# Performance work log

Hardware: AMD Instinct MI355X
Metric: run time of the kernel (lower is better)

## Reference

```python
import jax, jax.numpy as jnp
import numpy as np

NUM_NODE = 50000
NUM_REL = 50
NUM_EDGE = 1_000_000
NUM_TRI = 2_000_000
HIDDEN = 64


def setup_inputs() -> dict:
    key = jax.random.key(0)
    ks = jax.random.split(key, 9)
    rel_emb = jax.random.normal(ks[0], (NUM_REL, HIDDEN), dtype=jnp.float32)
    W_msg = jax.random.normal(ks[1], (2 * HIDDEN, HIDDEN), dtype=jnp.float32) / np.sqrt(2 * HIDDEN)
    W_upd = jax.random.normal(ks[2], (2 * HIDDEN, HIDDEN), dtype=jnp.float32) / np.sqrt(2 * HIDDEN)
    src = jax.random.randint(ks[3], (NUM_EDGE,), 0, NUM_NODE, dtype=jnp.int64 if jax.config.jax_enable_x64 else jnp.int32)
    dst = jax.random.randint(ks[4], (NUM_EDGE,), 0, NUM_NODE, dtype=src.dtype)
    rel = jax.random.randint(ks[5], (NUM_EDGE,), 0, NUM_REL, dtype=src.dtype)
    edge_ab = jax.random.randint(ks[6], (NUM_TRI,), 0, NUM_EDGE, dtype=src.dtype)
    edge_bc = jax.random.randint(ks[7], (NUM_TRI,), 0, NUM_EDGE, dtype=src.dtype)
    edge_ac = jax.random.randint(ks[8], (NUM_TRI,), 0, NUM_EDGE, dtype=src.dtype)
    return {
        "rel_emb": rel_emb, "W_msg": W_msg, "W_upd": W_upd,
        "src": src, "dst": dst, "rel": rel,
        "edge_ab": edge_ab, "edge_bc": edge_bc, "edge_ac": edge_ac,
    }


def reference(rel_emb, W_msg, W_upd, src, dst, rel, edge_ab, edge_bc, edge_ac):
    # Per-edge hidden state from relation embedding: [E, D]
    h = rel_emb[rel]
    num_edge = h.shape[0]
    # Triangle message: combine the two body edges of each grounding. [T, 2D]
    pair = jnp.concatenate([h[edge_ab], h[edge_bc]], axis=-1)
    msg = jax.nn.relu(pair @ W_msg)  # [T, D]
    # Scatter-add messages onto the head edge (a,c): irregular, memory-bound.
    agg = jax.ops.segment_sum(msg, edge_ac, num_segments=num_edge)  # [E, D]
    # Edge update.
    out = jax.nn.relu(jnp.concatenate([h, agg], axis=-1) @ W_upd)  # [E, D]
    return out
```

## Files before the change

kernel.cpp:

```cpp
#include <hip/hip_runtime.h>

#define HIDDEN 64
#define NREL 50
#define NPAIR (NREL * NREL)
#define BEDGE 64
#define CAP 512

typedef int   iv4 __attribute__((ext_vector_type(4)));
typedef float fv4 __attribute__((ext_vector_type(4)));

__global__ void precompute_tables(const float* __restrict__ rel_emb,
                                  const float* __restrict__ W_msg,
                                  const float* __restrict__ W_upd,
                                  const int* __restrict__ rel,
                                  unsigned char* __restrict__ rel8,
                                  int conv_n,
                                  float* __restrict__ M2,
                                  float* __restrict__ Hc) {
    const int p = blockIdx.x;
    const int j = threadIdx.x;

    for (int i = p * HIDDEN + j; i < conv_n; i += NPAIR * HIDDEN)
        rel8[i] = (unsigned char)rel[i];

    const int ra = p / NREL, rb = p % NREL;
    __shared__ float msg[HIDDEN];
    const float* ha = rel_emb + ra * HIDDEN;
    const float* hb = rel_emb + rb * HIDDEN;

    float acc = 0.f;
    #pragma unroll 8
    for (int i = 0; i < HIDDEN; ++i) acc += ha[i] * W_msg[i * HIDDEN + j];
    #pragma unroll 8
    for (int i = 0; i < HIDDEN; ++i) acc += hb[i] * W_msg[(HIDDEN + i) * HIDDEN + j];
    msg[j] = fmaxf(acc, 0.f);
    __syncthreads();

    float acc2 = 0.f;
    #pragma unroll 8
    for (int k = 0; k < HIDDEN; ++k) acc2 += msg[k] * W_upd[(HIDDEN + k) * HIDDEN + j];
    M2[p * HIDDEN + j] = acc2;

    if (p < NREL) {
        float acc3 = 0.f;
        #pragma unroll 8
        for (int i = 0; i < HIDDEN; ++i) acc3 += rel_emb[p * HIDDEN + i] * W_upd[i * HIDDEN + j];
        Hc[p * HIDDEN + j] = acc3;
    }
}

__global__ __launch_bounds__(256) void partition_tri(
        const unsigned char* __restrict__ rel8,
        const int* __restrict__ edge_ab,
        const int* __restrict__ edge_bc,
        const int* __restrict__ edge_ac,
        unsigned int* __restrict__ cur,
        unsigned int* __restrict__ buf,
        int num_tri) {
    const int n8 = num_tri >> 3;
    int i = blockIdx.x * blockDim.x + threadIdx.x;
    const int stride = gridDim.x * blockDim.x;
    for (; i < n8; i += stride) {
        const iv4 a0 = __builtin_nontemporal_load((const iv4*)edge_ab + 2 * i);
        const iv4 a1 = __builtin_nontemporal_load((const iv4*)edge_ab + 2 * i + 1);
        const iv4 b0 = __builtin_nontemporal_load((const iv4*)edge_bc + 2 * i);
        const iv4 b1 = __builtin_nontemporal_load((const iv4*)edge_bc + 2 * i + 1);
        const iv4 c0 = __builtin_nontemporal_load((const iv4*)edge_ac + 2 * i);
        const iv4 c1 = __builtin_nontemporal_load((const iv4*)edge_ac + 2 * i + 1);
        int p[8], c[8];
        #pragma unroll
        for (int k = 0; k < 4; ++k) {
            p[k]     = (int)rel8[a0[k]] * NREL + (int)rel8[b0[k]];
            p[k + 4] = (int)rel8[a1[k]] * NREL + (int)rel8[b1[k]];
            c[k]     = c0[k];
            c[k + 4] = c1[k];
        }
        unsigned int r[8];
        #pragma unroll
        for (int k = 0; k < 8; ++k)
            r[k] = atomicAdd(&cur[c[k] >> 6], 1u);
        #pragma unroll
        for (int k = 0; k < 8; ++k)
            if (r[k] < CAP)
                buf[(size_t)(c[k] >> 6) * CAP + r[k]] =
                    ((unsigned int)p[k] << 6) | ((unsigned int)c[k] & 63u);
    }
    const int rem = num_tri & 7;
    if (rem && blockIdx.x == gridDim.x - 1 && threadIdx.x < rem) {
        const int t = (num_tri & ~7) + threadIdx.x;
        const int p = (int)rel8[edge_ab[t]] * NREL + (int)rel8[edge_bc[t]];
        const int c = edge_ac[t];
        const unsigned int r = atomicAdd(&cur[c >> 6], 1u);
        if (r < CAP)
            buf[(size_t)(c >> 6) * CAP + r] =
                ((unsigned int)p << 6) | ((unsigned int)c & 63u);
    }
}

__global__ __launch_bounds__(256) void accumulate_bucket(
        const unsigned char* __restrict__ rel8,
        const unsigned int* __restrict__ cur,
        const unsigned int* __restrict__ buf,
        const float* __restrict__ M2,
        const float* __restrict__ Hc,
        float* __restrict__ out, int num_edge) {
    __shared__ unsigned int lk[CAP];
    const int b = blockIdx.x;
    const unsigned int craw = cur[b];
    const int cnt = craw < CAP ? (int)craw : CAP;
    for (int t = threadIdx.x; t < cnt; t += 256)
        lk[t] = buf[(size_t)b * CAP + t];
    __syncthreads();

    const int g     = threadIdx.x >> 4;
    const int l     = threadIdx.x & 15;
    const int shift = threadIdx.x & 48;

    for (int le = g; le < BEDGE; le += 16) {
        const int e = b * BEDGE + le;
        if (e >= num_edge) continue;
        const int re = rel8[e];
        fv4 acc = ((const fv4*)(Hc + re * HIDDEN))[l];
        for (int base = 0; base < cnt; base += 16) {
            const int idx = base + l;
            const unsigned int key = (idx < cnt) ? lk[idx] : 0u;
            const bool m = (idx < cnt) && ((int)(key & 63u) == le);
            const unsigned long long bal = __ballot(m);
            unsigned int mask = (unsigned int)((bal >> shift) & 0xFFFFull);
            while (mask) {
                const int bit = __ffs(mask) - 1;
                mask &= mask - 1;
                const int p = __shfl((int)(key >> 6), bit, 16);
                acc += ((const fv4*)M2)[p * 16 + l];
            }
        }
        fv4 o = acc;
        o.x = fmaxf(o.x, 0.f);
        o.y = fmaxf(o.y, 0.f);
        o.z = fmaxf(o.z, 0.f);
        o.w = fmaxf(o.w, 0.f);
        __builtin_nontemporal_store(o, (fv4*)out + (size_t)e * 16 + l);
    }
}

__global__ void scatter_tri(const int* __restrict__ rel,
                            const int* __restrict__ edge_ab,
                            const int* __restrict__ edge_bc,
                            const int* __restrict__ edge_ac,
                            const float* __restrict__ M2,
                            float* __restrict__ out, int num_tri) {
    const int lane   = threadIdx.x & 63;
    const int wave   = (int)((blockIdx.x * blockDim.x + threadIdx.x) >> 6);
    const int nwaves = (int)((gridDim.x * blockDim.x) >> 6);
    for (int t = wave; t < num_tri; t += nwaves) {
        const int p = rel[edge_ab[t]] * NREL + rel[edge_bc[t]];
        const float v = M2[p * HIDDEN + lane];
        unsafeAtomicAdd(&out[(size_t)edge_ac[t] * HIDDEN + lane], v);
    }
}

__global__ void finalize(const int* __restrict__ rel,
                         const float* __restrict__ Hc,
                         float* __restrict__ out, int num_edge) {
    const int total = num_edge * (HIDDEN / 4);
    int i = blockIdx.x * blockDim.x + threadIdx.x;
    const int stride = gridDim.x * blockDim.x;
    for (; i < total; i += stride) {
        const int e = i >> 4;
        const int q = i & 15;
        float4 a = ((const float4*)out)[i];
        float4 h = ((const float4*)(Hc + rel[e] * HIDDEN))[q];
        float4 o;
        o.x = fmaxf(a.x + h.x, 0.f);
        o.y = fmaxf(a.y + h.y, 0.f);
        o.z = fmaxf(a.z + h.z, 0.f);
        o.w = fmaxf(a.w + h.w, 0.f);
        ((float4*)out)[i] = o;
    }
}

extern "C" void kernel_launch(void* const* d_in, const int* in_sizes, int n_in,
                              void* d_out, int out_size, void* d_ws, size_t ws_size,
                              hipStream_t stream) {
    const float* rel_emb = (const float*)d_in[0];
    const float* W_msg   = (const float*)d_in[1];
    const float* W_upd   = (const float*)d_in[2];
    const int* rel     = (const int*)d_in[5];
    const int* edge_ab = (const int*)d_in[6];
    const int* edge_bc = (const int*)d_in[7];
    const int* edge_ac = (const int*)d_in[8];
    float* out = (float*)d_out;

    const int num_edge = in_sizes[5];
    const int num_tri  = in_sizes[6];
    const int NB = (num_edge + BEDGE - 1) / BEDGE;

    char* ws = (char*)d_ws;
    size_t off = 0;
    auto alloc = [&](size_t bytes) { char* p = ws + off; off = (off + bytes + 255) & ~(size_t)255; return p; };
    float*         M2   = (float*)alloc((size_t)NPAIR * HIDDEN * 4);
    float*         Hc   = (float*)alloc((size_t)NREL * HIDDEN * 4);
    unsigned char* rel8 = (unsigned char*)alloc((size_t)num_edge);
    unsigned int*  cur  = (unsigned int*)alloc((size_t)NB * 4);
    unsigned int*  buf  = (unsigned int*)alloc((size_t)NB * CAP * 4);
    const size_t required = off;

    const bool fast = (ws_size >= required);

    if (fast) {
        hipMemsetAsync(cur, 0, (size_t)NB * 4, stream);
        precompute_tables<<<NPAIR, HIDDEN, 0, stream>>>(rel_emb, W_msg, W_upd,
                                                        rel, rel8, num_edge, M2, Hc);
        const int n8 = num_tri >> 3;
        int pblocks = (n8 + 255) / 256;
        if (pblocks < 1) pblocks = 1;
        partition_tri<<<pblocks, 256, 0, stream>>>(rel8, edge_ab, edge_bc, edge_ac,
                                                   cur, buf, num_tri);
        accumulate_bucket<<<NB, 256, 0, stream>>>(rel8, cur, buf, M2, Hc,
                                                  out, num_edge);
    } else {
        precompute_tables<<<NPAIR, HIDDEN, 0, stream>>>(rel_emb, W_msg, W_upd,
                                                        rel, (unsigned char*)d_ws, 0, M2, Hc);
        hipMemsetAsync(d_out, 0, (size_t)out_size * sizeof(float), stream);
        scatter_tri<<<8192, 256, 0, stream>>>(rel, edge_ab, edge_bc, edge_ac, M2, out, num_tri);
        const int total4 = num_edge * (HIDDEN / 4);
        int fin_blocks = (total4 + 255) / 256;
        if (fin_blocks > 65535 * 8) fin_blocks = 65535 * 8;
        finalize<<<fin_blocks, 256, 0, stream>>>(rel, Hc, out, num_edge);
    }
}
```

Baseline: 465.4 us.

## Accumulate bucketed triangle messages with LDS atomics instead of ballot scans

The per-bucket accumulation kernel now keeps a padded shared-memory accumulator for all 64 edges in the bucket, seeded from the Hc table. Each group of 16 threads takes one bucketed key and adds the matching M2 row with LDS float atomics. This replaces the earlier scheme in which every edge group rescanned the whole key list with ballots and shuffles, doing work proportional to edges times keys. Bucket buffer writes and reads also switch to nontemporal accesses. The cost is a larger LDS footprint and contention among LDS atomics.

```diff
diff --git a/kernel.cpp b/kernel.cpp
--- a/kernel.cpp
+++ b/kernel.cpp
@@ -5,6 +5,7 @@
 #define NPAIR (NREL * NREL)
 #define BEDGE 64
 #define CAP 512
+#define AC_STRIDE 68
 
 typedef int   iv4 __attribute__((ext_vector_type(4)));
 typedef float fv4 __attribute__((ext_vector_type(4)));
@@ -82,8 +83,9 @@
         #pragma unroll
         for (int k = 0; k < 8; ++k)
             if (r[k] < CAP)
-                buf[(size_t)(c[k] >> 6) * CAP + r[k]] =
-                    ((unsigned int)p[k] << 6) | ((unsigned int)c[k] & 63u);
+                __builtin_nontemporal_store(
+                    ((unsigned int)p[k] << 6) | ((unsigned int)c[k] & 63u),
+                    &buf[(size_t)(c[k] >> 6) * CAP + r[k]]);
     }
     const int rem = num_tri & 7;
     if (rem && blockIdx.x == gridDim.x - 1 && threadIdx.x < rem) {
@@ -97,49 +99,54 @@
     }
 }
 
-__global__ __launch_bounds__(256) void accumulate_bucket(
+__global__ __launch_bounds__(256) void accumulate_lds(
         const unsigned char* __restrict__ rel8,
         const unsigned int* __restrict__ cur,
         const unsigned int* __restrict__ buf,
         const float* __restrict__ M2,
         const float* __restrict__ Hc,
         float* __restrict__ out, int num_edge) {
+    __shared__ float acc[BEDGE * AC_STRIDE];
     __shared__ unsigned int lk[CAP];
-    const int b = blockIdx.x;
+    const int b  = blockIdx.x;
+    const int e0 = b * BEDGE;
+    int ne = num_edge - e0;
+    if (ne > BEDGE) ne = BEDGE;
+
+    for (int idx = threadIdx.x; idx < ne * 16; idx += 256) {
+        const int le = idx >> 4, q = idx & 15;
+        const int re = rel8[e0 + le];
+        *(fv4*)(acc + le * AC_STRIDE + q * 4) = ((const fv4*)(Hc + re * HIDDEN))[q];
+    }
     const unsigned int craw = cur[b];
     const int cnt = craw < CAP ? (int)craw : CAP;
     for (int t = threadIdx.x; t < cnt; t += 256)
-        lk[t] = buf[(size_t)b * CAP + t];
+        lk[t] = __builtin_nontemporal_load(buf + (size_t)b * CAP + t);
     __syncthreads();
 
-    const int g     = threadIdx.x >> 4;
-    const int l     = threadIdx.x & 15;
-    const int shift = threadIdx.x & 48;
-
-    for (int le = g; le < BEDGE; le += 16) {
-        const int e = b * BEDGE + le;
-        if (e >= num_edge) continue;
-        const int re = rel8[e];
-        fv4 acc = ((const fv4*)(Hc + re * HIDDEN))[l];
-        for (int base = 0; base < cnt; base += 16) {
-            const int idx = base + l;
-            const unsigned int key = (idx < cnt) ? lk[idx] : 0u;
-            const bool m = (idx < cnt) && ((int)(key & 63u) == le);
-            const unsigned long long bal = __ballot(m);
-            unsigned int mask = (unsigned int)((bal >> shift) & 0xFFFFull);
-            while (mask) {
-                const int bit = __ffs(mask) - 1;
-                mask &= mask - 1;
-                const int p = __shfl((int)(key >> 6), bit, 16);
-                acc += ((const fv4*)M2)[p * 16 + l];
-            }
-        }
-        fv4 o = acc;
-        o.x = fmaxf(o.x, 0.f);
-        o.y = fmaxf(o.y, 0.f);
-        o.z = fmaxf(o.z, 0.f);
-        o.w = fmaxf(o.w, 0.f);
-        __builtin_nontemporal_store(o, (fv4*)out + (size_t)e * 16 + l);
+    const int g = threadIdx.x >> 4;
+    const int l = threadIdx.x & 15;
+    for (int kidx = g; kidx < cnt; kidx += 16) {
+        const unsigned int key = lk[kidx];
+        const int le = (int)(key & 63u);
+        const int p  = (int)(key >> 6);
+        const fv4 m = ((const fv4*)M2)[p * 16 + l];
+        float* dst = acc + le * AC_STRIDE + l * 4;
+        atomicAdd(dst + 0, m.x);
+        atomicAdd(dst + 1, m.y);
+        atomicAdd(dst + 2, m.z);
+        atomicAdd(dst + 3, m.w);
+    }
+    __syncthreads();
+
+    for (int idx = threadIdx.x; idx < ne * 16; idx += 256) {
+        const int le = idx >> 4, q = idx & 15;
+        fv4 v = *(const fv4*)(acc + le * AC_STRIDE + q * 4);
+        v.x = fmaxf(v.x, 0.f);
+        v.y = fmaxf(v.y, 0.f);
+        v.z = fmaxf(v.z, 0.f);
+        v.w = fmaxf(v.w, 0.f);
+        __builtin_nontemporal_store(v, (fv4*)out + (size_t)(e0 + le) * 16 + q);
     }
 }
 
@@ -216,8 +223,8 @@
         if (pblocks < 1) pblocks = 1;
         partition_tri<<<pblocks, 256, 0, stream>>>(rel8, edge_ab, edge_bc, edge_ac,
                                                    cur, buf, num_tri);
-        accumulate_bucket<<<NB, 256, 0, stream>>>(rel8, cur, buf, M2, Hc,
-                                                  out, num_edge);
+        accumulate_lds<<<NB, 256, 0, stream>>>(rel8, cur, buf, M2, Hc,
+                                               out, num_edge);
     } else {
         precompute_tables<<<NPAIR, HIDDEN, 0, stream>>>(rel_emb, W_msg, W_upd,
                                                         rel, (unsigned char*)d_ws, 0, M2, Hc);
```

Result: slower. 1.051 ms (+125.8%).

## Fuse precompute, partition and accumulate into one cooperative persistent kernel

Applied to the files above, without the earlier changes.

Replaces the memset plus three kernel launches with a single cooperative kernel. It zeroes counters, converts rel, builds the pair tables, partitions triangles into buckets and accumulates per-edge outputs, with grid-wide syncs between phases. The aim is to remove launch gaps and inter-kernel idle time. The cost is that a grid-sync barrier and a persistent grid capped at 2048 blocks may reduce latency hiding in the memory-bound phases. It falls back to the old multi-kernel path if the cooperative launch fails.

```diff
diff --git a/kernel.cpp b/kernel.cpp
--- a/kernel.cpp
+++ b/kernel.cpp
@@ -1,4 +1,7 @@
 #include <hip/hip_runtime.h>
+#include <hip/hip_cooperative_groups.h>
+
+namespace cg = cooperative_groups;
 
 #define HIDDEN 64
 #define NREL 50
@@ -8,6 +11,144 @@
 
 typedef int   iv4 __attribute__((ext_vector_type(4)));
 typedef float fv4 __attribute__((ext_vector_type(4)));
+
+__global__ __launch_bounds__(256) void fused_pipeline(
+        const float* __restrict__ rel_emb,
+        const float* __restrict__ W_msg,
+        const float* __restrict__ W_upd,
+        const int* __restrict__ rel,
+        const int* __restrict__ edge_ab,
+        const int* __restrict__ edge_bc,
+        const int* __restrict__ edge_ac,
+        unsigned char* __restrict__ rel8,
+        float* __restrict__ M2,
+        float* __restrict__ Hc,
+        unsigned int* __restrict__ cur,
+        unsigned int* __restrict__ buf,
+        float* __restrict__ out,
+        int num_edge, int num_tri, int NB_) {
+    cg::grid_group grid = cg::this_grid();
+    __shared__ float msg[4][HIDDEN];
+    __shared__ unsigned int lk[CAP];
+
+    const int tid      = threadIdx.x;
+    const int gtid     = blockIdx.x * blockDim.x + tid;
+    const int gthreads = gridDim.x * blockDim.x;
+
+    for (int i = gtid; i < NB_; i += gthreads) cur[i] = 0u;
+    for (int i = gtid; i < num_edge; i += gthreads) rel8[i] = (unsigned char)rel[i];
+
+    {
+        const int sub = tid >> 6;
+        const int j   = tid & 63;
+        const int pb  = blockIdx.x * 4 + sub;
+        if (pb < NPAIR) {
+            const int ra = pb / NREL, rb = pb % NREL;
+            const float* ha = rel_emb + ra * HIDDEN;
+            const float* hb = rel_emb + rb * HIDDEN;
+            float acc = 0.f;
+            #pragma unroll 8
+            for (int i = 0; i < HIDDEN; ++i) acc += ha[i] * W_msg[i * HIDDEN + j];
+            #pragma unroll 8
+            for (int i = 0; i < HIDDEN; ++i) acc += hb[i] * W_msg[(HIDDEN + i) * HIDDEN + j];
+            msg[sub][j] = fmaxf(acc, 0.f);
+            __syncthreads();
+            float acc2 = 0.f;
+            #pragma unroll 8
+            for (int k = 0; k < HIDDEN; ++k) acc2 += msg[sub][k] * W_upd[(HIDDEN + k) * HIDDEN + j];
+            M2[pb * HIDDEN + j] = acc2;
+            if (pb < NREL) {
+                float acc3 = 0.f;
+                #pragma unroll 8
+                for (int i = 0; i < HIDDEN; ++i) acc3 += rel_emb[pb * HIDDEN + i] * W_upd[i * HIDDEN + j];
+                Hc[pb * HIDDEN + j] = acc3;
+            }
+        }
+    }
+    grid.sync();
+
+    {
+        const int n8 = num_tri >> 3;
+        for (int i = gtid; i < n8; i += gthreads) {
+            const iv4 a0 = __builtin_nontemporal_load((const iv4*)edge_ab + 2 * i);
+            const iv4 a1 = __builtin_nontemporal_load((const iv4*)edge_ab + 2 * i + 1);
+            const iv4 b0 = __builtin_nontemporal_load((const iv4*)edge_bc + 2 * i);
+            const iv4 b1 = __builtin_nontemporal_load((const iv4*)edge_bc + 2 * i + 1);
+            const iv4 c0 = __builtin_nontemporal_load((const iv4*)edge_ac + 2 * i);
+            const iv4 c1 = __builtin_nontemporal_load((const iv4*)edge_ac + 2 * i + 1);
+            int p[8], c[8];
+            #pragma unroll
+            for (int k = 0; k < 4; ++k) {
+                p[k]     = (int)rel8[a0[k]] * NREL + (int)rel8[b0[k]];
+                p[k + 4] = (int)rel8[a1[k]] * NREL + (int)rel8[b1[k]];
+                c[k]     = c0[k];
+                c[k + 4] = c1[k];
+            }
+            unsigned int r[8];
+            #pragma unroll
+            for (int k = 0; k < 8; ++k)
+                r[k] = atomicAdd(&cur[c[k] >> 6], 1u);
+            #pragma unroll
+            for (int k = 0; k < 8; ++k)
+                if (r[k] < CAP)
+                    buf[(size_t)(c[k] >> 6) * CAP + r[k]] =
+                        ((unsigned int)p[k] << 6) | ((unsigned int)c[k] & 63u);
+        }
+        const int rem = num_tri & 7;
+        if (gtid < rem) {
+            const int t = (num_tri & ~7) + gtid;
+            const int p = (int)rel8[edge_ab[t]] * NREL + (int)rel8[edge_bc[t]];
+            const int c = edge_ac[t];
+            const unsigned int r = atomicAdd(&cur[c >> 6], 1u);
+            if (r < CAP)
+                buf[(size_t)(c >> 6) * CAP + r] =
+                    ((unsigned int)p << 6) | ((unsigned int)c & 63u);
+        }
+    }
+    grid.sync();
+
+    {
+        const int g     = tid >> 4;
+        const int l     = tid & 15;
+        const int shift = tid & 48;
+        for (int b = blockIdx.x; b < NB_; b += gridDim.x) {
+            const unsigned int craw = cur[b];
+            const int cnt = craw < CAP ? (int)craw : CAP;
+            for (int t = tid; t < cnt; t += 256)
+                lk[t] = buf[(size_t)b * CAP + t];
+            __syncthreads();
+
+            const int e0 = b * BEDGE;
+            for (int le = g; le < BEDGE; le += 16) {
+                const int e = e0 + le;
+                if (e < num_edge) {
+                    const int re = rel8[e];
+                    fv4 acc = ((const fv4*)(Hc + re * HIDDEN))[l];
+                    for (int base = 0; base < cnt; base += 16) {
+                        const int idx = base + l;
+                        const unsigned int key = (idx < cnt) ? lk[idx] : 0u;
+                        const bool m = (idx < cnt) && ((int)(key & 63u) == le);
+                        const unsigned long long bal = __ballot(m);
+                        unsigned int mask = (unsigned int)((bal >> shift) & 0xFFFFull);
+                        while (mask) {
+                            const int bit = __ffs(mask) - 1;
+                            mask &= mask - 1;
+                            const int p = __shfl((int)(key >> 6), bit, 16);
+                            acc += ((const fv4*)M2)[p * 16 + l];
+                        }
+                    }
+                    fv4 o = acc;
+                    o.x = fmaxf(o.x, 0.f);
+                    o.y = fmaxf(o.y, 0.f);
+                    o.z = fmaxf(o.z, 0.f);
+                    o.w = fmaxf(o.w, 0.f);
+                    __builtin_nontemporal_store(o, (fv4*)out + (size_t)e * 16 + l);
+                }
+            }
+            __syncthreads();
+        }
+    }
+}
 
 __global__ void precompute_tables(const float* __restrict__ rel_emb,
                                   const float* __restrict__ W_msg,
@@ -19,15 +160,12 @@
                                   float* __restrict__ Hc) {
     const int p = blockIdx.x;
     const int j = threadIdx.x;
-
     for (int i = p * HIDDEN + j; i < conv_n; i += NPAIR * HIDDEN)
         rel8[i] = (unsigned char)rel[i];
-
     const int ra = p / NREL, rb = p % NREL;
     __shared__ float msg[HIDDEN];
     const float* ha = rel_emb + ra * HIDDEN;
     const float* hb = rel_emb + rb * HIDDEN;
-
     float acc = 0.f;
     #pragma unroll 8
     for (int i = 0; i < HIDDEN; ++i) acc += ha[i] * W_msg[i * HIDDEN + j];
@@ -35,12 +173,10 @@
     for (int i = 0; i < HIDDEN; ++i) acc += hb[i] * W_msg[(HIDDEN + i) * HIDDEN + j];
     msg[j] = fmaxf(acc, 0.f);
     __syncthreads();
-
     float acc2 = 0.f;
     #pragma unroll 8
     for (int k = 0; k < HIDDEN; ++k) acc2 += msg[k] * W_upd[(HIDDEN + k) * HIDDEN + j];
     M2[p * HIDDEN + j] = acc2;
-
     if (p < NREL) {
         float acc3 = 0.f;
         #pragma unroll 8
@@ -111,11 +247,9 @@
     for (int t = threadIdx.x; t < cnt; t += 256)
         lk[t] = buf[(size_t)b * CAP + t];
     __syncthreads();
-
     const int g     = threadIdx.x >> 4;
     const int l     = threadIdx.x & 15;
     const int shift = threadIdx.x & 48;
-
     for (int le = g; le < BEDGE; le += 16) {
         const int e = b * BEDGE + le;
         if (e >= num_edge) continue;
@@ -193,7 +327,7 @@
 
     const int num_edge = in_sizes[5];
     const int num_tri  = in_sizes[6];
-    const int NB = (num_edge + BEDGE - 1) / BEDGE;
+    int NB = (num_edge + BEDGE - 1) / BEDGE;
 
     char* ws = (char*)d_ws;
     size_t off = 0;
@@ -205,19 +339,38 @@
     unsigned int*  buf  = (unsigned int*)alloc((size_t)NB * CAP * 4);
     const size_t required = off;
 
-    const bool fast = (ws_size >= required);
-
-    if (fast) {
-        hipMemsetAsync(cur, 0, (size_t)NB * 4, stream);
-        precompute_tables<<<NPAIR, HIDDEN, 0, stream>>>(rel_emb, W_msg, W_upd,
-                                                        rel, rel8, num_edge, M2, Hc);
-        const int n8 = num_tri >> 3;
-        int pblocks = (n8 + 255) / 256;
-        if (pblocks < 1) pblocks = 1;
-        partition_tri<<<pblocks, 256, 0, stream>>>(rel8, edge_ab, edge_bc, edge_ac,
-                                                   cur, buf, num_tri);
-        accumulate_bucket<<<NB, 256, 0, stream>>>(rel8, cur, buf, M2, Hc,
-                                                  out, num_edge);
+    if (ws_size >= required) {
+        bool launched = false;
+        int occ = 0;
+        hipError_t oe = hipOccupancyMaxActiveBlocksPerMultiprocessor(
+                            &occ, fused_pipeline, 256, 0);
+        if (oe == hipSuccess && occ > 0) {
+            int grid = occ * 256;
+            if (grid > 2048) grid = 2048;
+            void* args[] = {
+                (void*)&rel_emb, (void*)&W_msg, (void*)&W_upd, (void*)&rel,
+                (void*)&edge_ab, (void*)&edge_bc, (void*)&edge_ac,
+                (void*)&rel8, (void*)&M2, (void*)&Hc,
+                (void*)&cur, (void*)&buf, (void*)&out,
+                (void*)&num_edge, (void*)&num_tri, (void*)&NB };
+            hipError_t le = hipLaunchCooperativeKernel(
+                                (const void*)fused_pipeline,
+                                dim3(grid), dim3(256), args, 0, stream);
+            launched = (le == hipSuccess);
+        }
+        if (!launched) {
+            (void)hipGetLastError();
+            hipMemsetAsync(cur, 0, (size_t)NB * 4, stream);
+            precompute_tables<<<NPAIR, HIDDEN, 0, stream>>>(rel_emb, W_msg, W_upd,
+                                                            rel, rel8, num_edge, M2, Hc);
+            const int n8 = num_tri >> 3;
+            int pblocks = (n8 + 255) / 256;
+            if (pblocks < 1) pblocks = 1;
+            partition_tri<<<pblocks, 256, 0, stream>>>(rel8, edge_ab, edge_bc, edge_ac,
+                                                       cur, buf, num_tri);
+            accumulate_bucket<<<NB, 256, 0, stream>>>(rel8, cur, buf, M2, Hc,
+                                                      out, num_edge);
+        }
     } else {
         precompute_tables<<<NPAIR, HIDDEN, 0, stream>>>(rel_emb, W_msg, W_upd,
                                                         rel, (unsigned char*)d_ws, 0, M2, Hc);
```

After: 782.7 us. 68.2% more time.
